# Kernel optimization log

Hardware: AMD Instinct MI355X
Metric: run time of the kernel (lower is better)

Reference implementation:

```python
import jax, jax.numpy as jnp
import numpy as np

B, L, H, DK, DV, DM = 8, 1024, 8, 80, 80, 640
LN_EPS = 1e-5


def setup_inputs() -> dict:
    key = jax.random.key(0)
    ks = jax.random.split(key, 5)
    q = jax.random.normal(ks[0], (B, L, DM), dtype=jnp.float32)
    k = jax.random.normal(ks[1], (B, L, DM), dtype=jnp.float32)
    v = jax.random.normal(ks[2], (B, L, DM), dtype=jnp.float32)
    # fc: nn.Linear(n_head*d_v, d_model), xavier-normal init
    fc_std = float(np.sqrt(2.0 / (H * DV + DM)))
    fc_w = jax.random.normal(ks[3], (DM, H * DV), dtype=jnp.float32) * fc_std
    fc_b = jnp.zeros((DM,), dtype=jnp.float32)
    gamma_1 = jnp.full((DM,), 1e-4, dtype=jnp.float32)  # init_values * ones(640)
    ln_w = jnp.ones((DM,), dtype=jnp.float32)
    ln_b = jnp.zeros((DM,), dtype=jnp.float32)
    return {"q": q, "k": k, "v": v, "fc_w": fc_w, "fc_b": fc_b,
            "gamma_1": gamma_1, "ln_w": ln_w, "ln_b": ln_b}


def reference(q, k, v, fc_w, fc_b, gamma_1, ln_w, ln_b):
    # Inputs are viewed directly into heads (projections are commented out in source).
    residual = q
    qh = q.reshape(B, L, H, DK)  # [b, q, h, d]
    kh = k.reshape(B, L, H, DK)  # [b, k, h, d]
    vh = v.reshape(B, L, H, DV)  # [b, k, h, d]

    # L2-distance attention scores: -sum((q-k)^2) = -(||q||^2 - 2 q.k + ||k||^2)
    sq = jnp.sum(qh * qh, axis=-1)                       # [b, q, h]
    sk = jnp.sum(kh * kh, axis=-1)                       # [b, k, h]
    cross = jnp.einsum('bqhd,bkhd->bhqk', qh, kh)        # [b, h, q, k]
    scores = -(sq.transpose(0, 2, 1)[:, :, :, None]
               - 2.0 * cross
               + sk.transpose(0, 2, 1)[:, :, None, :]) / 13.0

    attn = jax.nn.softmax(scores, axis=-1)               # softmax over keys (dim=2 in 3D view)
    # dropout(p=0.8) treated as identity (eval mode)

    out = jnp.einsum('bhqk,bkhd->bqhd', attn, vh)        # [b, q, h, dv]
    out = out.reshape(B, L, H * DV)
    out = out @ fc_w.T + fc_b                            # fc projection
    # dropout treated as identity (eval mode)

    x = out * gamma_1 + residual
    mu = jnp.mean(x, axis=-1, keepdims=True)
    var = jnp.mean((x - mu) ** 2, axis=-1, keepdims=True)
    y = (x - mu) * jax.lax.rsqrt(var + LN_EPS) * ln_w + ln_b
    return y
```

## Files before the change

### kernel.cpp

```cpp
#include <hip/hip_runtime.h>

#define B_ 8
#define L_ 1024
#define H_ 8
#define DM_ 640

typedef __attribute__((ext_vector_type(8))) short bf16x8;
typedef __attribute__((ext_vector_type(4))) short bf16x4;
typedef __attribute__((ext_vector_type(4))) float f32x4;
typedef __attribute__((ext_vector_type(2))) float f32x2;
typedef __attribute__((ext_vector_type(2))) int i32x2;
typedef __attribute__((ext_vector_type(4))) int i32x4;
typedef __attribute__((ext_vector_type(4))) unsigned short us4;
typedef __attribute__((ext_vector_type(8))) unsigned short us8;

#if __has_builtin(__builtin_amdgcn_exp2f)
#define EXP2F __builtin_amdgcn_exp2f
#else
#define EXP2F exp2f
#endif

#define C1F 0.22195308f
#define C2F 0.11097654f

#define VTP_TILE_SHORTS 5184
#define ATTN8_OFF 10616832

__device__ __forceinline__ unsigned short f2bf(float f) {
  unsigned int u = __builtin_bit_cast(unsigned int, f);
  u += 0x7fffu + ((u >> 16) & 1u);
  return (unsigned short)(u >> 16);
}
__device__ __forceinline__ float bf2f(unsigned short h) {
  unsigned int u = ((unsigned int)h) << 16;
  return __builtin_bit_cast(float, u);
}
__device__ __forceinline__ float sane(float x, float lim) {
  return fminf(fmaxf(x, -lim), lim);
}
__device__ __forceinline__ unsigned cvt_pk_bf16(float a, float b) {
  unsigned r;
  asm("v_cvt_pk_bf16_f32 %0, %1, %2" : "=v"(r) : "v"(a), "v"(b));
  return r;
}

__global__ __launch_bounds__(256) void prep_kernel(
    const float* __restrict__ kg, const float* __restrict__ vg,
    unsigned short* __restrict__ Kp, unsigned short* __restrict__ Vtp) {
  __shared__ float V_lds[64 * 81];
  __shared__ float w_lds[64];
  const int tid = threadIdx.x;
  const int bh = blockIdx.x >> 4, kt = blockIdx.x & 15;
  const int b = bh >> 3, h = bh & 7;
  const int key = tid >> 2, part = tid & 3;
  const int keyg = kt * 64 + key;

  const float* krow = kg + (size_t)(b * L_ + keyg) * DM_ + h * 80 + part * 20;
  const float* vrow = vg + (size_t)(b * L_ + keyg) * DM_ + h * 80 + part * 20;
  unsigned short* kpr = Kp + ((size_t)bh * L_ + keyg) * 80 + part * 20;

  float ssq = 0.f;
#pragma unroll
  for (int i = 0; i < 5; ++i) {
    float4 f = *(const float4*)(krow + 4 * i);
    ssq += f.x * f.x + f.y * f.y + f.z * f.z + f.w * f.w;
    us4 h4 = {f2bf(f.x * C1F), f2bf(f.y * C1F), f2bf(f.z * C1F), f2bf(f.w * C1F)};
    *(us4*)(kpr + 4 * i) = h4;
    float4 g4 = *(const float4*)(vrow + 4 * i);
    int d0 = part * 20 + 4 * i;
    V_lds[key * 81 + d0 + 0] = g4.x;
    V_lds[key * 81 + d0 + 1] = g4.y;
    V_lds[key * 81 + d0 + 2] = g4.z;
    V_lds[key * 81 + d0 + 3] = g4.w;
  }
  ssq += __shfl_xor(ssq, 1);
  ssq += __shfl_xor(ssq, 2);
  if (part == 0) w_lds[key] = EXP2F((80.f - ssq) * C2F);
  __syncthreads();

  unsigned short* vt = Vtp + (size_t)(bh * 16 + kt) * VTP_TILE_SHORTS;
#pragma unroll
  for (int r = 0; r < 11; ++r) {
    int p = r * 256 + tid;
    if (p < 81 * 32) {
      int dv = p >> 5, kp = (p & 31) * 2;
      float wa = w_lds[kp], wb = w_lds[kp + 1];
      float va = (dv < 80) ? V_lds[kp * 81 + dv] * wa : wa;
      float vb = (dv < 80) ? V_lds[(kp + 1) * 81 + dv] * wb : wb;
      *(unsigned*)(vt + dv * 64 + kp) =
          (unsigned)f2bf(va) | ((unsigned)f2bf(vb) << 16);
    }
  }
}

#define KSTR 104
#define VSTR 76

__global__ __launch_bounds__(128) void attn_kernel(
    const float* __restrict__ qg, const unsigned short* __restrict__ Kp,
    const unsigned short* __restrict__ Vtp, unsigned char* __restrict__ attn8) {
  __shared__ __align__(16) unsigned short K_lds[64 * KSTR];
  __shared__ __align__(16) unsigned short Vt_lds[80 * VSTR];
  __shared__ __align__(16) unsigned short w_sh[64];

  const int tid = threadIdx.x;
  const int wid = tid >> 6, lane = tid & 63;
  const int col = lane & 15, g = lane >> 4;
  const int bx = blockIdx.x;
  const int bh = bx & 63, qt = bx >> 6;
  const int b = bh >> 3, h = bh & 7;

  if (tid < 64) {
    us8 z = {0, 0, 0, 0, 0, 0, 0, 0};
    *(us8*)&K_lds[tid * KSTR + 80] = z;
    *(us8*)&K_lds[tid * KSTR + 88] = z;
  }

  int krr[5], kcc[5], vrr[5], vcc[5];
#pragma unroll
  for (int i = 0; i < 5; ++i) {
    int f = tid + 128 * i;
    krr[i] = f / 10;
    kcc[i] = f - krr[i] * 10;
    vrr[i] = f >> 3;
    vcc[i] = f & 7;
  }
  const unsigned short* kslice = Kp + (size_t)bh * L_ * 80;
  const unsigned short* vslice = Vtp + (size_t)(bh * 16) * VTP_TILE_SHORTS;

  us8 sk[5], sv[5], sw;
  auto load_tile = [&](int kt) {
    const unsigned short* kb = kslice + (size_t)kt * 5120;
    const unsigned short* vb = vslice + (size_t)kt * VTP_TILE_SHORTS;
#pragma unroll
    for (int i = 0; i < 5; ++i) {
      sk[i] = *(const us8*)(kb + krr[i] * 80 + kcc[i] * 8);
      sv[i] = *(const us8*)(vb + vrr[i] * 64 + vcc[i] * 8);
    }
    if (tid < 8) sw = *(const us8*)(vb + 5120 + tid * 8);
  };
  auto write_tile = [&]() {
#pragma unroll
    for (int i = 0; i < 5; ++i) {
      *(us8*)&K_lds[krr[i] * KSTR + kcc[i] * 8] = sk[i];
      *(us8*)&Vt_lds[vrr[i] * VSTR + vcc[i] * 8] = sv[i];
    }
    if (tid < 8) *(us8*)&w_sh[tid * 8] = sw;
  };

  bf16x8 qa0[3], qa1[3];
  {
    const int qr0 = qt * 64 + wid * 16 + col;
#pragma unroll
    for (int s = 0; s < 2; ++s) {
      const float* qr = qg + (size_t)(b * L_ + qr0 + s * 32) * DM_ + h * 80;
      bf16x8* qa = s ? qa1 : qa0;
#pragma unroll
      for (int c = 0; c < 3; ++c) {
        int d0 = c * 32 + g * 8;
        if (d0 < 80) {
          float4 f0 = *(const float4*)(qr + d0);
          float4 f1 = *(const float4*)(qr + d0 + 4);
          qa[c][0] = (short)f2bf(f0.x); qa[c][1] = (short)f2bf(f0.y);
          qa[c][2] = (short)f2bf(f0.z); qa[c][3] = (short)f2bf(f0.w);
          qa[c][4] = (short)f2bf(f1.x); qa[c][5] = (short)f2bf(f1.y);
          qa[c][6] = (short)f2bf(f1.z); qa[c][7] = (short)f2bf(f1.w);
        } else {
#pragma unroll
          for (int e = 0; e < 8; ++e) qa[c][e] = 0;
        }
      }
    }
  }

  f32x4 acc_o0[5], acc_o1[5];
#pragma unroll
  for (int u = 0; u < 5; ++u) {
    f32x4 z = {0.f, 0.f, 0.f, 0.f};
    acc_o0[u] = z;
    acc_o1[u] = z;
  }
  float lp0 = 0.f, lp1 = 0.f;

  load_tile(0);

  for (int kt = 0; kt < 16; ++kt) {
    __syncthreads();
    write_tile();
    __syncthreads();
    if (kt < 15) load_tile(kt + 1);

    f32x4 accS0[4], accS1[4];
#pragma unroll
    for (int t = 0; t < 4; ++t) {
      f32x4 z = {0.f, 0.f, 0.f, 0.f};
      accS0[t] = z;
      accS1[t] = z;
    }
#pragma unroll
    for (int t = 0; t < 4; ++t)
#pragma unroll
      for (int c = 0; c < 3; ++c) {
        bf16x8 kf = *(const bf16x8*)&K_lds[(t * 16 + col) * KSTR + c * 32 + g * 8];
        accS0[t] = __builtin_amdgcn_mfma_f32_16x16x32_bf16(kf, qa0[c], accS0[t], 0, 0, 0);
        accS1[t] = __builtin_amdgcn_mfma_f32_16x16x32_bf16(kf, qa1[c], accS1[t], 0, 0, 0);
      }

#pragma unroll
    for (int t = 0; t < 4; ++t) {
      us4 w4 = *(const us4*)&w_sh[t * 16 + g * 4];
      float w0 = bf2f(w4[0]), w1 = bf2f(w4[1]), w2 = bf2f(w4[2]), w3 = bf2f(w4[3]);
      float p00 = EXP2F(accS0[t][0]), p01 = EXP2F(accS0[t][1]);
      float p02 = EXP2F(accS0[t][2]), p03 = EXP2F(accS0[t][3]);
      float p10 = EXP2F(accS1[t][0]), p11 = EXP2F(accS1[t][1]);
      float p12 = EXP2F(accS1[t][2]), p13 = EXP2F(accS1[t][3]);
      lp0 += p00 * w0 + p01 * w1 + p02 * w2 + p03 * w3;
      lp1 += p10 * w0 + p11 * w1 + p12 * w2 + p13 * w3;
      i32x2 pw0 = {(int)cvt_pk_bf16(p00, p01), (int)cvt_pk_bf16(p02, p03)};
      i32x2 pw1 = {(int)cvt_pk_bf16(p10, p11), (int)cvt_pk_bf16(p12, p13)};
      bf16x4 pf0 = __builtin_bit_cast(bf16x4, pw0);
      bf16x4 pf1 = __builtin_bit_cast(bf16x4, pw1);
#pragma unroll
      for (int u = 0; u < 5; ++u) {
        bf16x4 vf = *(const bf16x4*)&Vt_lds[(u * 16 + col) * VSTR + t * 16 + g * 4];
        acc_o0[u] = __builtin_amdgcn_mfma_f32_16x16x16bf16_1k(vf, pf0, acc_o0[u], 0, 0, 0);
        acc_o1[u] = __builtin_amdgcn_mfma_f32_16x16x16bf16_1k(vf, pf1, acc_o1[u], 0, 0, 0);
      }
    }
  }

  float l0 = lp0 + __shfl_xor(lp0, 16);
  l0 += __shfl_xor(l0, 32);
  float l1 = lp1 + __shfl_xor(lp1, 16);
  l1 += __shfl_xor(l1, 32);
#pragma unroll
  for (int s = 0; s < 2; ++s) {
    f32x4* acc_o = s ? acc_o1 : acc_o0;
    float invl = 1.0f / fmaxf(s ? l1 : l0, 1e-30f);
    const int qrow = qt * 64 + s * 32 + wid * 16 + col;
    unsigned char* ob = attn8 + (size_t)(b * L_ + qrow) * DM_ + h * 80;
#pragma unroll
    for (int u = 0; u < 5; ++u) {
      float o0 = sane(acc_o[u][0] * invl, 240.f);
      float o1 = sane(acc_o[u][1] * invl, 240.f);
      float o2 = sane(acc_o[u][2] * invl, 240.f);
      float o3 = sane(acc_o[u][3] * invl, 240.f);
      int pk = __builtin_amdgcn_cvt_pk_fp8_f32(o0, o1, 0, false);
      pk = __builtin_amdgcn_cvt_pk_fp8_f32(o2, o3, pk, true);
      *(int*)(ob + u * 16 + g * 4) = pk;
    }
  }
}

#define BSTR 40
__global__ __launch_bounds__(256) void fc_kernel(
    const unsigned char* __restrict__ attn8, const float* __restrict__ w,
    const float* __restrict__ fcb, const float* __restrict__ gamma,
    const float* __restrict__ qres, unsigned short* __restrict__ xout) {
  __shared__ __align__(16) unsigned short A_lds[2][128 * BSTR];
  __shared__ __align__(16) unsigned short B_lds[2][128 * BSTR];

  const int tid = threadIdx.x;
  const int wid = tid >> 6, lane = tid & 63;
  const int col = lane & 15, g = lane >> 4;
  const int rt = blockIdx.x / 5, ct = blockIdx.x % 5;
  const int wm = wid >> 1, wn = wid & 1;
  const int r = tid >> 1, seg = tid & 1;

  f32x4 acc[4][4];
#pragma unroll
  for (int m = 0; m < 4; ++m)
#pragma unroll
    for (int n = 0; n < 4; ++n) {
      f32x4 z = {0.f, 0.f, 0.f, 0.f};
      acc[m][n] = z;
    }

  uint4 sa;
  float4 sb[4];
  auto load_k = [&](int kc) {
    sa = *(const uint4*)(attn8 + (size_t)(rt * 128 + r) * DM_ + kc * 32 + seg * 16);
    const float* wsrc = w + (size_t)(ct * 128 + r) * DM_ + kc * 32 + seg * 16;
#pragma unroll
    for (int i = 0; i < 4; ++i) sb[i] = *(const float4*)(wsrc + 4 * i);
  };
  auto write_k = [&](int bf) {
    const unsigned* adw = (const unsigned*)&sa;
#pragma unroll
    for (int wde = 0; wde < 4; ++wde) {
      f32x2 lo = __builtin_amdgcn_cvt_pk_f32_fp8(adw[wde], false);
      f32x2 hi = __builtin_amdgcn_cvt_pk_f32_fp8(adw[wde], true);
      us4 h4 = {f2bf(lo[0]), f2bf(lo[1]), f2bf(hi[0]), f2bf(hi[1])};
      *(us4*)&A_lds[bf][r * BSTR + seg * 16 + wde * 4] = h4;
    }
#pragma unroll
    for (int i = 0; i < 4; ++i) {
      us4 h4 = {f2bf(sb[i].x), f2bf(sb[i].y), f2bf(sb[i].z), f2bf(sb[i].w)};
      *(us4*)&B_lds[bf][r * BSTR + seg * 16 + 4 * i] = h4;
    }
  };

  load_k(0);
  write_k(0);
  __syncthreads();

  for (int kc = 0; kc < 20; ++kc) {
    const int cur = kc & 1;
    if (kc < 19) load_k(kc + 1);

    bf16x8 af[4], bfr[4];
#pragma unroll
    for (int m = 0; m < 4; ++m)
      af[m] = *(const bf16x8*)&A_lds[cur][(wm * 64 + m * 16 + col) * BSTR + g * 8];
#pragma unroll
    for (int n = 0; n < 4; ++n)
      bfr[n] = *(const bf16x8*)&B_lds[cur][(wn * 64 + n * 16 + col) * BSTR + g * 8];
#pragma unroll
    for (int m = 0; m < 4; ++m)
#pragma unroll
      for (int n = 0; n < 4; ++n)
        acc[m][n] = __builtin_amdgcn_mfma_f32_16x16x32_bf16(af[m], bfr[n], acc[m][n], 0, 0, 0);

    if (kc < 19) {
      write_k(cur ^ 1);
      __syncthreads();
    }
  }

  int jcol[4];
  float fb4[4], gm[4];
#pragma unroll
  for (int n = 0; n < 4; ++n) {
    jcol[n] = ct * 128 + wn * 64 + n * 16 + col;
    fb4[n] = fcb[jcol[n]];
    gm[n] = gamma[jcol[n]];
  }
#pragma unroll
  for (int m = 0; m < 4; ++m) {
    int rowg = rt * 128 + wm * 64 + m * 16 + g * 4;
#pragma unroll
    for (int j = 0; j < 4; ++j) {
      int row = rowg + j;
#pragma unroll
      for (int n = 0; n < 4; ++n) {
        float xv = (acc[m][n][j] + fb4[n]) * gm[n] + qres[(size_t)row * DM_ + jcol[n]];
        xout[(size_t)row * DM_ + jcol[n]] = f2bf(sane(xv, 1e5f));
      }
    }
  }
}

__global__ __launch_bounds__(256) void ln_kernel(
    const unsigned short* __restrict__ x, const float* __restrict__ lw,
    const float* __restrict__ lb, float* __restrict__ y) {
  const int wid = threadIdx.x >> 6, lane = threadIdx.x & 63;
  const int row = blockIdx.x * 4 + wid;
  const unsigned short* xr = x + (size_t)row * DM_;

  unsigned int u[5];
  float s = 0.f, ss = 0.f;
#pragma unroll
  for (int i = 0; i < 5; ++i) {
    u[i] = *(const unsigned int*)(xr + 2 * (lane + 64 * i));
    float a0 = bf2f((unsigned short)(u[i] & 0xffff));
    float a1 = bf2f((unsigned short)(u[i] >> 16));
    s += a0 + a1;
    ss += a0 * a0 + a1 * a1;
  }
#pragma unroll
  for (int d = 1; d < 64; d <<= 1) {
    s += __shfl_xor(s, d);
    ss += __shfl_xor(ss, d);
  }
  const float mu = s * (1.f / 640.f);
  const float var = ss * (1.f / 640.f) - mu * mu;
  const float rstd = rsqrtf(var + 1e-5f);

  float* yr = y + (size_t)row * DM_;
#pragma unroll
  for (int i = 0; i < 5; ++i) {
    int c0 = 2 * (lane + 64 * i);
    float a0 = bf2f((unsigned short)(u[i] & 0xffff));
    float a1 = bf2f((unsigned short)(u[i] >> 16));
    float2 wv = *(const float2*)(lw + c0);
    float2 bv = *(const float2*)(lb + c0);
    float2 out;
    out.x = (a0 - mu) * rstd * wv.x + bv.x;
    out.y = (a1 - mu) * rstd * wv.y + bv.y;
    *(float2*)(yr + c0) = out;
  }
}

extern "C" void kernel_launch(void* const* d_in, const int* in_sizes, int n_in,
                              void* d_out, int out_size, void* d_ws, size_t ws_size,
                              hipStream_t stream) {
  const float* q = (const float*)d_in[0];
  const float* k = (const float*)d_in[1];
  const float* v = (const float*)d_in[2];
  const float* fw = (const float*)d_in[3];
  const float* fb = (const float*)d_in[4];
  const float* g1 = (const float*)d_in[5];
  const float* lw = (const float*)d_in[6];
  const float* lb = (const float*)d_in[7];

  unsigned short* vtp = (unsigned short*)d_out;
  unsigned char* attn8 = (unsigned char*)d_out + ATTN8_OFF;
  unsigned short* kp = (unsigned short*)d_ws;
  unsigned short* xws = (unsigned short*)d_ws;
  float* y = (float*)d_out;

  prep_kernel<<<dim3(64 * 16), dim3(256), 0, stream>>>(k, v, kp, vtp);
  attn_kernel<<<dim3(64 * 16), dim3(128), 0, stream>>>(q, kp, vtp, attn8);
  fc_kernel<<<dim3((8192 / 128) * 5), dim3(256), 0, stream>>>(attn8, fw, fb, g1, q, xws);
  ln_kernel<<<dim3(8192 / 4), dim3(256), 0, stream>>>(xws, lw, lb, y);
}
```

Measured before the change: 94.08 us.

## Double-buffer attention K/V tiles, widen attention blocks, and shrink FC tiles

The attention kernel moves to 256-thread blocks covering 128 query rows each. It double-buffers the K/Vt/w tiles in LDS so the next tile's global load and LDS write overlap compute with a single barrier per iteration, and wraps the MFMA sections in s_setprio. The FC GEMM switches from 128x128 to 64x64 output tiles, giving four times as many blocks for better CU occupancy, and packs bf16 conversions into wider LDS stores. The costs are twice the LDS per attention block and more redundant global reads of the FC weights and activations, since reuse per tile is lower.

After: 84.01 us. 10.7% less time.

```diff
diff --git a/kernel.cpp b/kernel.cpp
--- a/kernel.cpp
+++ b/kernel.cpp
@@ -10,7 +10,6 @@
 typedef __attribute__((ext_vector_type(4))) float f32x4;
 typedef __attribute__((ext_vector_type(2))) float f32x2;
 typedef __attribute__((ext_vector_type(2))) int i32x2;
-typedef __attribute__((ext_vector_type(4))) int i32x4;
 typedef __attribute__((ext_vector_type(4))) unsigned short us4;
 typedef __attribute__((ext_vector_type(8))) unsigned short us8;
 
@@ -96,12 +95,12 @@
 #define KSTR 104
 #define VSTR 76
 
-__global__ __launch_bounds__(128) void attn_kernel(
+__global__ __launch_bounds__(256, 2) void attn_kernel(
     const float* __restrict__ qg, const unsigned short* __restrict__ Kp,
     const unsigned short* __restrict__ Vtp, unsigned char* __restrict__ attn8) {
-  __shared__ __align__(16) unsigned short K_lds[64 * KSTR];
-  __shared__ __align__(16) unsigned short Vt_lds[80 * VSTR];
-  __shared__ __align__(16) unsigned short w_sh[64];
+  __shared__ __align__(16) unsigned short K_lds[2][64 * KSTR];
+  __shared__ __align__(16) unsigned short Vt_lds[2][80 * VSTR];
+  __shared__ __align__(16) unsigned short w_sh[2][64];
 
   const int tid = threadIdx.x;
   const int wid = tid >> 6, lane = tid & 63;
@@ -110,50 +109,52 @@
   const int bh = bx & 63, qt = bx >> 6;
   const int b = bh >> 3, h = bh & 7;
 
-  if (tid < 64) {
+  if (tid < 128) {
     us8 z = {0, 0, 0, 0, 0, 0, 0, 0};
-    *(us8*)&K_lds[tid * KSTR + 80] = z;
-    *(us8*)&K_lds[tid * KSTR + 88] = z;
-  }
-
-  int krr[5], kcc[5], vrr[5], vcc[5];
-#pragma unroll
-  for (int i = 0; i < 5; ++i) {
-    int f = tid + 128 * i;
-    krr[i] = f / 10;
-    kcc[i] = f - krr[i] * 10;
-    vrr[i] = f >> 3;
-    vcc[i] = f & 7;
-  }
+    int bufz = tid >> 6, r = tid & 63;
+    *(us8*)&K_lds[bufz][r * KSTR + 80] = z;
+    *(us8*)&K_lds[bufz][r * KSTR + 88] = z;
+  }
+
+  const int ka0 = tid, ka1 = tid + 256, ka2 = tid + 512;
+  const int kr0 = ka0 / 10, kc0 = ka0 - kr0 * 10;
+  const int kr1 = ka1 / 10, kc1 = ka1 - kr1 * 10;
+  const int kr2 = ka2 / 10, kc2 = ka2 - kr2 * 10;
+  const int vr0 = ka0 >> 3, vc0 = ka0 & 7;
+  const int vr1 = ka1 >> 3, vc1 = ka1 & 7;
+  const int vr2 = ka2 >> 3, vc2 = ka2 & 7;
+
   const unsigned short* kslice = Kp + (size_t)bh * L_ * 80;
   const unsigned short* vslice = Vtp + (size_t)(bh * 16) * VTP_TILE_SHORTS;
 
-  us8 sk[5], sv[5], sw;
+  us8 sk0, sk1, sk2, sv0, sv1, sv2, sw;
   auto load_tile = [&](int kt) {
     const unsigned short* kb = kslice + (size_t)kt * 5120;
     const unsigned short* vb = vslice + (size_t)kt * VTP_TILE_SHORTS;
-#pragma unroll
-    for (int i = 0; i < 5; ++i) {
-      sk[i] = *(const us8*)(kb + krr[i] * 80 + kcc[i] * 8);
-      sv[i] = *(const us8*)(vb + vrr[i] * 64 + vcc[i] * 8);
-    }
+    sk0 = *(const us8*)(kb + kr0 * 80 + kc0 * 8);
+    sk1 = *(const us8*)(kb + kr1 * 80 + kc1 * 8);
+    if (tid < 128) sk2 = *(const us8*)(kb + kr2 * 80 + kc2 * 8);
+    sv0 = *(const us8*)(vb + vr0 * 64 + vc0 * 8);
+    sv1 = *(const us8*)(vb + vr1 * 64 + vc1 * 8);
+    if (tid < 128) sv2 = *(const us8*)(vb + vr2 * 64 + vc2 * 8);
     if (tid < 8) sw = *(const us8*)(vb + 5120 + tid * 8);
   };
-  auto write_tile = [&]() {
-#pragma unroll
-    for (int i = 0; i < 5; ++i) {
-      *(us8*)&K_lds[krr[i] * KSTR + kcc[i] * 8] = sk[i];
-      *(us8*)&Vt_lds[vrr[i] * VSTR + vcc[i] * 8] = sv[i];
-    }
-    if (tid < 8) *(us8*)&w_sh[tid * 8] = sw;
+  auto write_tile = [&](int bf) {
+    *(us8*)&K_lds[bf][kr0 * KSTR + kc0 * 8] = sk0;
+    *(us8*)&K_lds[bf][kr1 * KSTR + kc1 * 8] = sk1;
+    if (tid < 128) *(us8*)&K_lds[bf][kr2 * KSTR + kc2 * 8] = sk2;
+    *(us8*)&Vt_lds[bf][vr0 * VSTR + vc0 * 8] = sv0;
+    *(us8*)&Vt_lds[bf][vr1 * VSTR + vc1 * 8] = sv1;
+    if (tid < 128) *(us8*)&Vt_lds[bf][vr2 * VSTR + vc2 * 8] = sv2;
+    if (tid < 8) *(us8*)&w_sh[bf][tid * 8] = sw;
   };
 
   bf16x8 qa0[3], qa1[3];
   {
-    const int qr0 = qt * 64 + wid * 16 + col;
+    const int qr0 = qt * 128 + wid * 16 + col;
 #pragma unroll
     for (int s = 0; s < 2; ++s) {
-      const float* qr = qg + (size_t)(b * L_ + qr0 + s * 32) * DM_ + h * 80;
+      const float* qr = qg + (size_t)(b * L_ + qr0 + s * 64) * DM_ + h * 80;
       bf16x8* qa = s ? qa1 : qa0;
 #pragma unroll
       for (int c = 0; c < 3; ++c) {
@@ -183,11 +184,11 @@
   float lp0 = 0.f, lp1 = 0.f;
 
   load_tile(0);
+  write_tile(0);
+  __syncthreads();
 
   for (int kt = 0; kt < 16; ++kt) {
-    __syncthreads();
-    write_tile();
-    __syncthreads();
+    const int cur = kt & 1;
     if (kt < 15) load_tile(kt + 1);
 
     f32x4 accS0[4], accS1[4];
@@ -197,18 +198,20 @@
       accS0[t] = z;
       accS1[t] = z;
     }
+    __builtin_amdgcn_s_setprio(1);
 #pragma unroll
     for (int t = 0; t < 4; ++t)
 #pragma unroll
       for (int c = 0; c < 3; ++c) {
-        bf16x8 kf = *(const bf16x8*)&K_lds[(t * 16 + col) * KSTR + c * 32 + g * 8];
+        bf16x8 kf = *(const bf16x8*)&K_lds[cur][(t * 16 + col) * KSTR + c * 32 + g * 8];
         accS0[t] = __builtin_amdgcn_mfma_f32_16x16x32_bf16(kf, qa0[c], accS0[t], 0, 0, 0);
         accS1[t] = __builtin_amdgcn_mfma_f32_16x16x32_bf16(kf, qa1[c], accS1[t], 0, 0, 0);
       }
+    __builtin_amdgcn_s_setprio(0);
 
 #pragma unroll
     for (int t = 0; t < 4; ++t) {
-      us4 w4 = *(const us4*)&w_sh[t * 16 + g * 4];
+      us4 w4 = *(const us4*)&w_sh[cur][t * 16 + g * 4];
       float w0 = bf2f(w4[0]), w1 = bf2f(w4[1]), w2 = bf2f(w4[2]), w3 = bf2f(w4[3]);
       float p00 = EXP2F(accS0[t][0]), p01 = EXP2F(accS0[t][1]);
       float p02 = EXP2F(accS0[t][2]), p03 = EXP2F(accS0[t][3]);
@@ -220,12 +223,19 @@
       i32x2 pw1 = {(int)cvt_pk_bf16(p10, p11), (int)cvt_pk_bf16(p12, p13)};
       bf16x4 pf0 = __builtin_bit_cast(bf16x4, pw0);
       bf16x4 pf1 = __builtin_bit_cast(bf16x4, pw1);
+      __builtin_amdgcn_s_setprio(1);
 #pragma unroll
       for (int u = 0; u < 5; ++u) {
-        bf16x4 vf = *(const bf16x4*)&Vt_lds[(u * 16 + col) * VSTR + t * 16 + g * 4];
+        bf16x4 vf = *(const bf16x4*)&Vt_lds[cur][(u * 16 + col) * VSTR + t * 16 + g * 4];
         acc_o0[u] = __builtin_amdgcn_mfma_f32_16x16x16bf16_1k(vf, pf0, acc_o0[u], 0, 0, 0);
         acc_o1[u] = __builtin_amdgcn_mfma_f32_16x16x16bf16_1k(vf, pf1, acc_o1[u], 0, 0, 0);
       }
+      __builtin_amdgcn_s_setprio(0);
+    }
+
+    if (kt < 15) {
+      write_tile(cur ^ 1);
+      __syncthreads();
     }
   }
 
@@ -237,7 +247,7 @@
   for (int s = 0; s < 2; ++s) {
     f32x4* acc_o = s ? acc_o1 : acc_o0;
     float invl = 1.0f / fmaxf(s ? l1 : l0, 1e-30f);
-    const int qrow = qt * 64 + s * 32 + wid * 16 + col;
+    const int qrow = qt * 128 + s * 64 + wid * 16 + col;
     unsigned char* ob = attn8 + (size_t)(b * L_ + qrow) * DM_ + h * 80;
 #pragma unroll
     for (int u = 0; u < 5; ++u) {
@@ -257,47 +267,48 @@
     const unsigned char* __restrict__ attn8, const float* __restrict__ w,
     const float* __restrict__ fcb, const float* __restrict__ gamma,
     const float* __restrict__ qres, unsigned short* __restrict__ xout) {
-  __shared__ __align__(16) unsigned short A_lds[2][128 * BSTR];
-  __shared__ __align__(16) unsigned short B_lds[2][128 * BSTR];
+  __shared__ __align__(16) unsigned short A_lds[2][64 * BSTR];
+  __shared__ __align__(16) unsigned short B_lds[2][64 * BSTR];
 
   const int tid = threadIdx.x;
   const int wid = tid >> 6, lane = tid & 63;
   const int col = lane & 15, g = lane >> 4;
-  const int rt = blockIdx.x / 5, ct = blockIdx.x % 5;
+  const int rt = blockIdx.x / 10, cn = blockIdx.x % 10;
   const int wm = wid >> 1, wn = wid & 1;
-  const int r = tid >> 1, seg = tid & 1;
-
-  f32x4 acc[4][4];
-#pragma unroll
-  for (int m = 0; m < 4; ++m)
-#pragma unroll
-    for (int n = 0; n < 4; ++n) {
+  const int r = tid >> 2, sg = tid & 3;
+
+  f32x4 acc[2][2];
+#pragma unroll
+  for (int m = 0; m < 2; ++m)
+#pragma unroll
+    for (int n = 0; n < 2; ++n) {
       f32x4 z = {0.f, 0.f, 0.f, 0.f};
       acc[m][n] = z;
     }
 
-  uint4 sa;
-  float4 sb[4];
+  uint2 sa;
+  float4 sb0, sb1;
   auto load_k = [&](int kc) {
-    sa = *(const uint4*)(attn8 + (size_t)(rt * 128 + r) * DM_ + kc * 32 + seg * 16);
-    const float* wsrc = w + (size_t)(ct * 128 + r) * DM_ + kc * 32 + seg * 16;
-#pragma unroll
-    for (int i = 0; i < 4; ++i) sb[i] = *(const float4*)(wsrc + 4 * i);
+    sa = *(const uint2*)(attn8 + (size_t)(rt * 64 + r) * DM_ + kc * 32 + sg * 8);
+    const float* wsrc = w + (size_t)(cn * 64 + r) * DM_ + kc * 32 + sg * 8;
+    sb0 = *(const float4*)wsrc;
+    sb1 = *(const float4*)(wsrc + 4);
   };
   auto write_k = [&](int bf) {
     const unsigned* adw = (const unsigned*)&sa;
-#pragma unroll
-    for (int wde = 0; wde < 4; ++wde) {
-      f32x2 lo = __builtin_amdgcn_cvt_pk_f32_fp8(adw[wde], false);
-      f32x2 hi = __builtin_amdgcn_cvt_pk_f32_fp8(adw[wde], true);
-      us4 h4 = {f2bf(lo[0]), f2bf(lo[1]), f2bf(hi[0]), f2bf(hi[1])};
-      *(us4*)&A_lds[bf][r * BSTR + seg * 16 + wde * 4] = h4;
-    }
-#pragma unroll
-    for (int i = 0; i < 4; ++i) {
-      us4 h4 = {f2bf(sb[i].x), f2bf(sb[i].y), f2bf(sb[i].z), f2bf(sb[i].w)};
-      *(us4*)&B_lds[bf][r * BSTR + seg * 16 + 4 * i] = h4;
-    }
+    unsigned ow[4];
+#pragma unroll
+    for (int d = 0; d < 2; ++d) {
+      f32x2 lo = __builtin_amdgcn_cvt_pk_f32_fp8(adw[d], false);
+      f32x2 hi = __builtin_amdgcn_cvt_pk_f32_fp8(adw[d], true);
+      ow[2 * d] = cvt_pk_bf16(lo[0], lo[1]);
+      ow[2 * d + 1] = cvt_pk_bf16(hi[0], hi[1]);
+    }
+    *(uint4*)&A_lds[bf][r * BSTR + sg * 8] =
+        *(const uint4*)ow;
+    unsigned bw[4] = {cvt_pk_bf16(sb0.x, sb0.y), cvt_pk_bf16(sb0.z, sb0.w),
+                      cvt_pk_bf16(sb1.x, sb1.y), cvt_pk_bf16(sb1.z, sb1.w)};
+    *(uint4*)&B_lds[bf][r * BSTR + sg * 8] = *(const uint4*)bw;
   };
 
   load_k(0);
@@ -308,17 +319,17 @@
     const int cur = kc & 1;
     if (kc < 19) load_k(kc + 1);
 
-    bf16x8 af[4], bfr[4];
-#pragma unroll
-    for (int m = 0; m < 4; ++m)
-      af[m] = *(const bf16x8*)&A_lds[cur][(wm * 64 + m * 16 + col) * BSTR + g * 8];
-#pragma unroll
-    for (int n = 0; n < 4; ++n)
-      bfr[n] = *(const bf16x8*)&B_lds[cur][(wn * 64 + n * 16 + col) * BSTR + g * 8];
-#pragma unroll
-    for (int m = 0; m < 4; ++m)
-#pragma unroll
-      for (int n = 0; n < 4; ++n)
+    bf16x8 af[2], bfr[2];
+#pragma unroll
+    for (int m = 0; m < 2; ++m)
+      af[m] = *(const bf16x8*)&A_lds[cur][(wm * 32 + m * 16 + col) * BSTR + g * 8];
+#pragma unroll
+    for (int n = 0; n < 2; ++n)
+      bfr[n] = *(const bf16x8*)&B_lds[cur][(wn * 32 + n * 16 + col) * BSTR + g * 8];
+#pragma unroll
+    for (int m = 0; m < 2; ++m)
+#pragma unroll
+      for (int n = 0; n < 2; ++n)
         acc[m][n] = __builtin_amdgcn_mfma_f32_16x16x32_bf16(af[m], bfr[n], acc[m][n], 0, 0, 0);
 
     if (kc < 19) {
@@ -327,23 +338,23 @@
     }
   }
 
-  int jcol[4];
-  float fb4[4], gm[4];
-#pragma unroll
-  for (int n = 0; n < 4; ++n) {
-    jcol[n] = ct * 128 + wn * 64 + n * 16 + col;
-    fb4[n] = fcb[jcol[n]];
+  int jcol[2];
+  float fb2[2], gm[2];
+#pragma unroll
+  for (int n = 0; n < 2; ++n) {
+    jcol[n] = cn * 64 + wn * 32 + n * 16 + col;
+    fb2[n] = fcb[jcol[n]];
     gm[n] = gamma[jcol[n]];
   }
 #pragma unroll
-  for (int m = 0; m < 4; ++m) {
-    int rowg = rt * 128 + wm * 64 + m * 16 + g * 4;
+  for (int m = 0; m < 2; ++m) {
+    int rowg = rt * 64 + wm * 32 + m * 16 + g * 4;
 #pragma unroll
     for (int j = 0; j < 4; ++j) {
       int row = rowg + j;
 #pragma unroll
-      for (int n = 0; n < 4; ++n) {
-        float xv = (acc[m][n][j] + fb4[n]) * gm[n] + qres[(size_t)row * DM_ + jcol[n]];
+      for (int n = 0; n < 2; ++n) {
+        float xv = (acc[m][n][j] + fb2[n]) * gm[n] + qres[(size_t)row * DM_ + jcol[n]];
         xout[(size_t)row * DM_ + jcol[n]] = f2bf(sane(xv, 1e5f));
       }
     }
@@ -410,7 +421,7 @@
   float* y = (float*)d_out;
 
   prep_kernel<<<dim3(64 * 16), dim3(256), 0, stream>>>(k, v, kp, vtp);
-  attn_kernel<<<dim3(64 * 16), dim3(128), 0, stream>>>(q, kp, vtp, attn8);
-  fc_kernel<<<dim3((8192 / 128) * 5), dim3(256), 0, stream>>>(attn8, fw, fb, g1, q, xws);
+  attn_kernel<<<dim3(64 * 8), dim3(256), 0, stream>>>(q, kp, vtp, attn8);
+  fc_kernel<<<dim3(128 * 10), dim3(256), 0, stream>>>(attn8, fw, fb, g1, q, xws);
   ln_kernel<<<dim3(8192 / 4), dim3(256), 0, stream>>>(xws, lw, lb, y);
 }
```
